# Optimization experiments

Measured on AMD Instinct MI355X. Metric: run time of the kernel, lower is better.

Reference implementation:

```python
import jax, jax.numpy as jnp
import numpy as np

H = 32       # total query heads
HK = 8       # kv heads (GQA)
D = 128      # head_dim = hidden // H
HIDDEN = 4096
THETA = 10000.0


def setup_inputs() -> dict:
    key = jax.random.key(0)
    k1, k2, k3 = jax.random.split(key, 3)
    B, S = 2, 2048
    positions = jnp.arange(S, dtype=jnp.int32)
    hidden_states = jax.random.normal(k1, (B, S, HIDDEN), dtype=jnp.float32)
    w_qkv = jax.random.normal(k2, (HIDDEN, (H + 2 * HK) * D), dtype=jnp.float32) * 0.02
    w_o = jax.random.normal(k3, (H * D, HIDDEN), dtype=jnp.float32) * 0.02
    return {"positions": positions, "hidden_states": hidden_states,
            "w_qkv": w_qkv, "w_o": w_o}


def _rope(x, cos, sin):
    # neox-style rotary: split halves, rotate
    x1, x2 = jnp.split(x, 2, axis=-1)
    return jnp.concatenate([x1 * cos - x2 * sin, x2 * cos + x1 * sin], axis=-1)


def reference(positions, hidden_states, w_qkv, w_o):
    B, S, _ = hidden_states.shape
    qkv = hidden_states @ w_qkv                        # [B,S,(H+2HK)*D]
    q, k, v = jnp.split(qkv, [H * D, H * D + HK * D], axis=-1)
    q = q.reshape(B, S, H, D)
    k = k.reshape(B, S, HK, D)
    v = v.reshape(B, S, HK, D)

    inv_freq = 1.0 / (THETA ** (jnp.arange(0, D, 2, dtype=jnp.float32) / D))
    freqs = positions.astype(jnp.float32)[:, None] * inv_freq[None, :]  # [S,D/2]
    cos = jnp.cos(freqs)[None, :, None, :]
    sin = jnp.sin(freqs)[None, :, None, :]
    q = _rope(q, cos, sin)
    k = _rope(k, cos, sin)

    G = H // HK  # query heads per kv head
    qg = q.reshape(B, S, HK, G, D)
    scores = jnp.einsum('bqhgd,bkhd->bhgqk', qg, k) * (D ** -0.5)
    causal = jnp.tril(jnp.ones((S, S), dtype=bool))
    scores = jnp.where(causal[None, None, None], scores, jnp.float32(-1e30))
    probs = jax.nn.softmax(scores, axis=-1)
    out = jnp.einsum('bhgqk,bkhd->bqhgd', probs, v).reshape(B, S, H * D)
    return out @ w_o
```

## Files before the change

kernel.cpp:

```cpp
#include <hip/hip_runtime.h>

typedef unsigned short ushort_t;
typedef __attribute__((ext_vector_type(8))) short short8;
typedef __attribute__((ext_vector_type(4))) unsigned short ushort4_t;
typedef __attribute__((ext_vector_type(4))) float f32x4;

#define NH 32
#define NHK 8
#define HD 128
#define HID 4096
#define NB 2
#define SEQ 2048
#define NQKV ((NH + 2 * NHK) * HD)

static __device__ inline ushort_t f2bu(float x) {
  unsigned u = __builtin_bit_cast(unsigned, x);
  unsigned r = (u + 0x7FFFu + ((u >> 16) & 1u)) >> 16;
  return (ushort_t)r;
}

typedef __attribute__((address_space(1))) void gvoid;
typedef __attribute__((address_space(3))) void lvoid;
static __device__ inline void gld16(const void* g, void* l) {
  __builtin_amdgcn_global_load_lds((gvoid*)g, (lvoid*)l, 16, 0, 0);
}

__global__ void rope_tab_k(const int* __restrict__ positions, float* __restrict__ tab) {
  int i = blockIdx.x * 256 + threadIdx.x;
  int s = i >> 6, d = i & 63;
  float pos = (float)positions[s];
  float f = pos * exp2f(-0.20762050593046014f * (float)d);
  tab[2 * i] = cosf(f);
  tab[2 * i + 1] = sinf(f);
}

__global__ void h2b_k(const float* __restrict__ in, ushort_t* __restrict__ out) {
  long i = ((long)blockIdx.x * 256 + threadIdx.x) * 8;
  f32x4 a = *(const f32x4*)&in[i];
  f32x4 b = *(const f32x4*)&in[i + 4];
  ushort4_t ya, yb;
#pragma unroll
  for (int u = 0; u < 4; ++u) { ya[u] = f2bu(a[u]); yb[u] = f2bu(b[u]); }
  *(ushort4_t*)&out[i] = ya;
  *(ushort4_t*)&out[i + 4] = yb;
}

__global__ void wt_k(const float* __restrict__ in, ushort_t* __restrict__ out,
                     int K, int N) {
  __shared__ ushort_t T[64][72];
  int n0 = blockIdx.x * 64, k0 = blockIdx.y * 64;
  int t = threadIdx.x;
  int kr = t >> 4, nc = (t & 15) * 4;
#pragma unroll
  for (int p = 0; p < 4; ++p) {
    int k = kr + p * 16;
    f32x4 x = *(const f32x4*)&in[(long)(k0 + k) * N + n0 + nc];
    ushort4_t y;
#pragma unroll
    for (int u = 0; u < 4; ++u) y[u] = f2bu(x[u]);
    *(ushort4_t*)&T[k][nc] = y;
  }
  __syncthreads();
  int n = t >> 2, kc = (t & 3) * 16;
  ushort_t tmp[16];
#pragma unroll
  for (int j = 0; j < 16; ++j) tmp[j] = T[kc + j][n];
  *(short8*)&out[(long)(n0 + n) * K + k0 + kc] = *(short8*)&tmp[0];
  *(short8*)&out[(long)(n0 + n) * K + k0 + kc + 8] = *(short8*)&tmp[8];
}

template <int MODE>
__global__ __launch_bounds__(256, 2)
void gemm_bt(const ushort_t* __restrict__ A,
             const ushort_t* __restrict__ Bt,
             float* __restrict__ C,
             const float* __restrict__ tab,
             ushort_t* __restrict__ Qo,
             ushort_t* __restrict__ Ko,
             ushort_t* __restrict__ Vo,
             int M, int N, int K) {
  __shared__ ushort_t As[2][128 * 32];
  __shared__ ushort_t Bs[2][128 * 32];
  int m0 = blockIdx.y * 128, n0 = blockIdx.x * 128;
  int tid = threadIdx.x;
  int lane = tid & 63, wave = tid >> 6;
  int wm = wave * 32;
  int l15 = lane & 15, quad = lane >> 4;
  f32x4 acc[2][8];
#pragma unroll
  for (int i = 0; i < 2; ++i)
#pragma unroll
    for (int j = 0; j < 8; ++j) acc[i][j] = (f32x4){0.f, 0.f, 0.f, 0.f};

  int iw = wave * 2;
  int r0 = iw * 16 + (lane >> 2);
  int gk0 = ((lane & 3) ^ ((r0 >> 1) & 3)) * 8;
  int r1 = r0 + 16;
  int gk1 = ((lane & 3) ^ ((r1 >> 1) & 3)) * 8;

#define STAGE(buf, k0)                                                   \
  do {                                                                   \
    gld16(&A[(long)(m0 + r0) * K + (k0) + gk0], &As[buf][iw * 512]);     \
    gld16(&Bt[(long)(n0 + r0) * K + (k0) + gk0], &Bs[buf][iw * 512]);    \
    gld16(&A[(long)(m0 + r1) * K + (k0) + gk1], &As[buf][iw * 512 + 512]); \
    gld16(&Bt[(long)(n0 + r1) * K + (k0) + gk1], &Bs[buf][iw * 512 + 512]); \
  } while (0)

  int NT = K >> 5;
  STAGE(0, 0);
  __syncthreads();
  int cur = 0;
  for (int t = 0; t < NT; ++t) {
    if (t + 1 < NT) STAGE(cur ^ 1, (t + 1) << 5);
    short8 af[2], bfr[8];
#pragma unroll
    for (int i = 0; i < 2; ++i) {
      int r = wm + i * 16 + l15;
      af[i] = *(short8*)&As[cur][r * 32 + ((quad ^ ((r >> 1) & 3)) << 3)];
    }
#pragma unroll
    for (int j = 0; j < 8; ++j) {
      int r = j * 16 + l15;
      bfr[j] = *(short8*)&Bs[cur][r * 32 + ((quad ^ ((r >> 1) & 3)) << 3)];
    }
#pragma unroll
    for (int i = 0; i < 2; ++i)
#pragma unroll
      for (int j = 0; j < 8; ++j)
        acc[i][j] = __builtin_amdgcn_mfma_f32_16x16x32_bf16(af[i], bfr[j], acc[i][j], 0, 0, 0);
    __syncthreads();
    cur ^= 1;
  }
#undef STAGE

  if (MODE == 0) {
#pragma unroll
    for (int i = 0; i < 2; ++i)
#pragma unroll
      for (int j = 0; j < 8; ++j)
#pragma unroll
        for (int r = 0; r < 4; ++r) {
          int row = m0 + wm + i * 16 + quad * 4 + r;
          int col = n0 + j * 16 + l15;
          C[(long)row * N + col] = acc[i][j][r];
        }
  } else {
    int head = n0 >> 7;
    const float2* tb = (const float2*)tab;
    if (head < NH + NHK) {
      bool isq = head < NH;
      ushort_t* dst = isq ? (Qo + (long)head * SEQ * HD)
                          : (Ko + (long)(head - NH) * SEQ * HD);
      float sc = isq ? 0.08838834764831845f : 1.0f;
#pragma unroll
      for (int i = 0; i < 2; ++i)
#pragma unroll
        for (int r = 0; r < 4; ++r) {
          int s = m0 + wm + i * 16 + quad * 4 + r;
#pragma unroll
          for (int j = 0; j < 4; ++j) {
            int d = j * 16 + l15;
            float2 cs = tb[s * 64 + d];
            float x1 = acc[i][j][r], x2 = acc[i][j + 4][r];
            dst[(long)s * HD + d] = f2bu((x1 * cs.x - x2 * cs.y) * sc);
            dst[(long)s * HD + d + 64] = f2bu((x2 * cs.x + x1 * cs.y) * sc);
          }
        }
    } else {
      int hk = head - NH - NHK;
      ushort_t* dst = Vo + (long)hk * HD * SEQ;
#pragma unroll
      for (int i = 0; i < 2; ++i)
#pragma unroll
        for (int j = 0; j < 8; ++j)
#pragma unroll
          for (int r = 0; r < 4; ++r) {
            int s = m0 + wm + i * 16 + quad * 4 + r;
            int d = j * 16 + l15;
            dst[(long)d * SEQ + s] = f2bu(acc[i][j][r]);
          }
    }
  }
}

template <int MODE, typename TA>
__global__ __launch_bounds__(256, 2)
void gemm_kn(const TA* __restrict__ A,
             const float* __restrict__ B,
             float* __restrict__ C,
             const float* __restrict__ tab,
             ushort_t* __restrict__ Qo,
             ushort_t* __restrict__ Ko,
             ushort_t* __restrict__ Vo,
             int M, int N, int K) {
  __shared__ ushort_t As[128][40];
  __shared__ ushort_t Bs[128 * 32];
  int m0 = blockIdx.y * 128, n0 = blockIdx.x * 128;
  int tid = threadIdx.x;
  int lane = tid & 63, wave = tid >> 6;
  int wm = wave * 32;
  int l15 = lane & 15, quad = lane >> 4;
  f32x4 acc[2][8];
#pragma unroll
  for (int i = 0; i < 2; ++i)
#pragma unroll
    for (int j = 0; j < 8; ++j) acc[i][j] = (f32x4){0.f, 0.f, 0.f, 0.f};

  for (int k0 = 0; k0 < K; k0 += 32) {
    __syncthreads();
    if constexpr (sizeof(TA) == 2) {
#pragma unroll
      for (int it = 0; it < 2; ++it) {
        int v = tid + it * 256;
        int row = v >> 2, kc = (v & 3) * 8;
        *(short8*)&As[row][kc] =
            *(const short8*)&A[(long)(m0 + row) * K + k0 + kc];
      }
    } else {
#pragma unroll
      for (int it = 0; it < 4; ++it) {
        int v = tid + it * 256;
        int row = v >> 3, kc = (v & 7) * 4;
        f32x4 x = *(const f32x4*)&A[(long)(m0 + row) * K + k0 + kc];
        ushort4_t y;
#pragma unroll
        for (int u = 0; u < 4; ++u) y[u] = f2bu(x[u]);
        *(ushort4_t*)&As[row][kc] = y;
      }
    }
#pragma unroll
    for (int it = 0; it < 4; ++it) {
      int v = tid + it * 256;
      int kr = v >> 5, nc = (v & 31) * 4;
      f32x4 x = *(const f32x4*)&B[(long)(k0 + kr) * N + n0 + nc];
      int kg = (kr >> 3) << 3, ke = kr & 7;
#pragma unroll
      for (int u = 0; u < 4; ++u) {
        int n = nc + u;
        Bs[n * 32 + ((kg ^ (((n >> 2) & 3) << 3))) + ke] = f2bu(x[u]);
      }
    }
    __syncthreads();
    short8 af[2], bfr[8];
#pragma unroll
    for (int i = 0; i < 2; ++i) af[i] = *(short8*)&As[wm + i * 16 + l15][quad * 8];
#pragma unroll
    for (int j = 0; j < 8; ++j) {
      int n = j * 16 + l15;
      bfr[j] = *(short8*)&Bs[n * 32 + ((quad ^ ((n >> 2) & 3)) << 3)];
    }
#pragma unroll
    for (int i = 0; i < 2; ++i)
#pragma unroll
      for (int j = 0; j < 8; ++j)
        acc[i][j] = __builtin_amdgcn_mfma_f32_16x16x32_bf16(af[i], bfr[j], acc[i][j], 0, 0, 0);
  }

  if (MODE == 0) {
#pragma unroll
    for (int i = 0; i < 2; ++i)
#pragma unroll
      for (int j = 0; j < 8; ++j)
#pragma unroll
        for (int r = 0; r < 4; ++r) {
          int row = m0 + wm + i * 16 + quad * 4 + r;
          int col = n0 + j * 16 + l15;
          C[(long)row * N + col] = acc[i][j][r];
        }
  } else {
    int head = n0 >> 7;
    const float2* tb = (const float2*)tab;
    if (head < NH + NHK) {
      bool isq = head < NH;
      ushort_t* dst = isq ? (Qo + (long)head * SEQ * HD)
                          : (Ko + (long)(head - NH) * SEQ * HD);
      float sc = isq ? 0.08838834764831845f : 1.0f;
#pragma unroll
      for (int i = 0; i < 2; ++i)
#pragma unroll
        for (int r = 0; r < 4; ++r) {
          int s = m0 + wm + i * 16 + quad * 4 + r;
#pragma unroll
          for (int j = 0; j < 4; ++j) {
            int d = j * 16 + l15;
            float2 cs = tb[s * 64 + d];
            float x1 = acc[i][j][r], x2 = acc[i][j + 4][r];
            dst[(long)s * HD + d] = f2bu((x1 * cs.x - x2 * cs.y) * sc);
            dst[(long)s * HD + d + 64] = f2bu((x2 * cs.x + x1 * cs.y) * sc);
          }
        }
    } else {
      int hk = head - NH - NHK;
      ushort_t* dst = Vo + (long)hk * HD * SEQ;
#pragma unroll
      for (int i = 0; i < 2; ++i)
#pragma unroll
        for (int j = 0; j < 8; ++j)
#pragma unroll
          for (int r = 0; r < 4; ++r) {
            int s = m0 + wm + i * 16 + quad * 4 + r;
            int d = j * 16 + l15;
            dst[(long)d * SEQ + s] = f2bu(acc[i][j][r]);
          }
    }
  }
}

__global__ __launch_bounds__(256, 2) void attn_k(const ushort_t* __restrict__ Q,
                                                 const ushort_t* __restrict__ Kg,
                                                 const ushort_t* __restrict__ Vt,
                                                 ushort_t* __restrict__ Aout) {
  __shared__ ushort_t Ks[64][136];
  __shared__ ushort_t Vs[128][72];
  __shared__ ushort_t Ps[4][16][72];
  int qt = ((int)gridDim.x - 1 - blockIdx.x) * 64;
  int h = blockIdx.y;
  int hk = h >> 2;
  const ushort_t* Qh = Q + (long)h * SEQ * HD;
  const ushort_t* Kh = Kg + (long)hk * SEQ * HD;
  const ushort_t* Vh = Vt + (long)hk * HD * SEQ;
  int tid = threadIdx.x, lane = tid & 63, wave = tid >> 6;
  int l15 = lane & 15, quad = lane >> 4;
  int qw = qt + wave * 16;
  short8 qf[4];
#pragma unroll
  for (int c = 0; c < 4; ++c)
    qf[c] = *(const short8*)&Qh[(long)(qw + l15) * HD + c * 32 + quad * 8];
  f32x4 O[8];
#pragma unroll
  for (int dt = 0; dt < 8; ++dt) O[dt] = (f32x4){0.f, 0.f, 0.f, 0.f};
  float mrow[4], lrow[4];
#pragma unroll
  for (int r = 0; r < 4; ++r) { mrow[r] = -1e30f; lrow[r] = 0.f; }
  int kend = qt + 64;
  for (int kc = 0; kc < kend; kc += 64) {
    __syncthreads();
#pragma unroll
    for (int i = 0; i < 4; ++i) {
      int v = tid + i * 256;
      int kr = v >> 4, dc = (v & 15) * 8;
      *(short8*)&Ks[kr][dc] = *(const short8*)&Kh[(long)(kc + kr) * HD + dc];
    }
#pragma unroll
    for (int i = 0; i < 4; ++i) {
      int v = tid + i * 256;
      int dr = v >> 3, kcol = (v & 7) * 8;
      *(short8*)&Vs[dr][kcol] = *(const short8*)&Vh[(long)dr * SEQ + kc + kcol];
    }
    __syncthreads();
    bool active = (kc <= qw + 15);
    if (active) {
      f32x4 S[4];
#pragma unroll
      for (int t = 0; t < 4; ++t) S[t] = (f32x4){0.f, 0.f, 0.f, 0.f};
#pragma unroll
      for (int c = 0; c < 4; ++c) {
#pragma unroll
        for (int t = 0; t < 4; ++t) {
          short8 kf = *(short8*)&Ks[t * 16 + l15][c * 32 + quad * 8];
          S[t] = __builtin_amdgcn_mfma_f32_16x16x32_bf16(qf[c], kf, S[t], 0, 0, 0);
        }
      }
#pragma unroll
      for (int r = 0; r < 4; ++r) {
        int qrow = qw + quad * 4 + r;
        float vv[4];
#pragma unroll
        for (int t = 0; t < 4; ++t)
          vv[t] = (kc + t * 16 + l15 <= qrow) ? S[t][r] : -1e30f;
        float mx = fmaxf(fmaxf(vv[0], vv[1]), fmaxf(vv[2], vv[3]));
        mx = fmaxf(mx, __shfl_xor(mx, 1, 64));
        mx = fmaxf(mx, __shfl_xor(mx, 2, 64));
        mx = fmaxf(mx, __shfl_xor(mx, 4, 64));
        mx = fmaxf(mx, __shfl_xor(mx, 8, 64));
        float mnew = fmaxf(mrow[r], mx);
        float alpha = __expf(mrow[r] - mnew);
        float p[4];
#pragma unroll
        for (int t = 0; t < 4; ++t) p[t] = __expf(vv[t] - mnew);
        float rs = (p[0] + p[1]) + (p[2] + p[3]);
        rs += __shfl_xor(rs, 1, 64);
        rs += __shfl_xor(rs, 2, 64);
        rs += __shfl_xor(rs, 4, 64);
        rs += __shfl_xor(rs, 8, 64);
        lrow[r] = lrow[r] * alpha + rs;
        mrow[r] = mnew;
#pragma unroll
        for (int dt = 0; dt < 8; ++dt) O[dt][r] *= alpha;
#pragma unroll
        for (int t = 0; t < 4; ++t)
          Ps[wave][quad * 4 + r][t * 16 + l15] = f2bu(p[t]);
      }
    }
    __syncthreads();
    if (active) {
      short8 pf0 = *(short8*)&Ps[wave][l15][quad * 8];
      short8 pf1 = *(short8*)&Ps[wave][l15][32 + quad * 8];
#pragma unroll
      for (int dt = 0; dt < 8; ++dt) {
        short8 vf0 = *(short8*)&Vs[dt * 16 + l15][quad * 8];
        short8 vf1 = *(short8*)&Vs[dt * 16 + l15][32 + quad * 8];
        O[dt] = __builtin_amdgcn_mfma_f32_16x16x32_bf16(pf0, vf0, O[dt], 0, 0, 0);
        O[dt] = __builtin_amdgcn_mfma_f32_16x16x32_bf16(pf1, vf1, O[dt], 0, 0, 0);
      }
    }
  }
#pragma unroll
  for (int dt = 0; dt < 8; ++dt)
#pragma unroll
    for (int r = 0; r < 4; ++r) {
      int q = qw + quad * 4 + r;
      float o = O[dt][r] / lrow[r];
      Aout[(long)q * (NH * HD) + h * HD + dt * 16 + l15] = f2bu(o);
    }
}

extern "C" void kernel_launch(void* const* d_in, const int* in_sizes, int n_in,
                              void* d_out, int out_size, void* d_ws, size_t ws_size,
                              hipStream_t stream) {
  const int* positions = (const int*)d_in[0];
  const float* hidden = (const float*)d_in[1];
  const float* w_qkv = (const float*)d_in[2];
  const float* w_o = (const float*)d_in[3];
  char* ws = (char*)d_ws;
  ushort_t* Qb = (ushort_t*)(ws + 0L);
  ushort_t* Kb = (ushort_t*)(ws + 16777216L);
  ushort_t* Vtb = (ushort_t*)(ws + 20971520L);
  ushort_t* attno = (ushort_t*)(ws + 25165824L);
  float* tab = (float*)attno;
  ushort_t* hb16 = (ushort_t*)(ws + 41943040L);
  ushort_t* wqkvT = (ushort_t*)(ws + 75497472L);
  ushort_t* woT = (ushort_t*)(ws + 125829120L);
  float* outf = (float*)d_out;
  bool big = ws_size >= 159383552ULL;

  if (big) {
    h2b_k<<<dim3((NB * SEQ * HID) / (256 * 8)), 256, 0, stream>>>(hidden, hb16);
    wt_k<<<dim3(NQKV / 64, HID / 64), 256, 0, stream>>>(w_qkv, wqkvT, HID, NQKV);
    wt_k<<<dim3(HID / 64, HID / 64), 256, 0, stream>>>(w_o, woT, HID, HID);
  }
  for (int b = 0; b < NB; ++b) {
    rope_tab_k<<<dim3((SEQ * 64) / 256), 256, 0, stream>>>(positions, tab);
    if (big) {
      gemm_bt<1><<<dim3(NQKV / 128, SEQ / 128), 256, 0, stream>>>(
          hb16 + (long)b * SEQ * HID, wqkvT, nullptr, tab, Qb, Kb, Vtb,
          SEQ, NQKV, HID);
    } else {
      gemm_kn<1, float><<<dim3(NQKV / 128, SEQ / 128), 256, 0, stream>>>(
          hidden + (long)b * SEQ * HID, w_qkv, nullptr, tab, Qb, Kb, Vtb,
          SEQ, NQKV, HID);
    }
    attn_k<<<dim3(SEQ / 64, NH), 256, 0, stream>>>(Qb, Kb, Vtb, attno);
    if (big) {
      gemm_bt<0><<<dim3(HID / 128, SEQ / 128), 256, 0, stream>>>(
          attno, woT, outf + (long)b * SEQ * HID, nullptr, nullptr, nullptr,
          nullptr, SEQ, HID, HID);
    } else {
      gemm_kn<0, ushort_t><<<dim3(HID / 128, SEQ / 128), 256, 0, stream>>>(
          attno, w_o, outf + (long)b * SEQ * HID, nullptr, nullptr, nullptr,
          nullptr, SEQ, HID, HID);
    }
  }
}
```

Before: 1.014 ms.

## Double-buffer K/V tile loads via registers and widen attention blocks to 128 queries

The attention kernel now runs 512 threads (8 waves) per block, covering 128 query rows, so each K/V tile staged in LDS serves twice as many queries. Global loads for the next K/V tile are prefetched into registers while the current tile is computed, then written to LDS at the start of the next iteration. MFMA sections are wrapped in s_setprio to favour matrix instructions. Register pressure rises from the two prefetch buffers, and with 128-row blocks the causal tail leaves more waves idle per block.

```diff
diff --git a/kernel.cpp b/kernel.cpp
--- a/kernel.cpp
+++ b/kernel.cpp
@@ -306,14 +306,14 @@
   }
 }
 
-__global__ __launch_bounds__(256, 2) void attn_k(const ushort_t* __restrict__ Q,
+__global__ __launch_bounds__(512, 2) void attn_k(const ushort_t* __restrict__ Q,
                                                  const ushort_t* __restrict__ Kg,
                                                  const ushort_t* __restrict__ Vt,
                                                  ushort_t* __restrict__ Aout) {
   __shared__ ushort_t Ks[64][136];
   __shared__ ushort_t Vs[128][72];
-  __shared__ ushort_t Ps[4][16][72];
-  int qt = ((int)gridDim.x - 1 - blockIdx.x) * 64;
+  __shared__ ushort_t Ps[8][16][72];
+  int qt = ((int)gridDim.x - 1 - blockIdx.x) * 128;
   int h = blockIdx.y;
   int hk = h >> 2;
   const ushort_t* Qh = Q + (long)h * SEQ * HD;
@@ -322,6 +322,28 @@
   int tid = threadIdx.x, lane = tid & 63, wave = tid >> 6;
   int l15 = lane & 15, quad = lane >> 4;
   int qw = qt + wave * 16;
+  int skr0 = tid >> 4, sdc0 = (tid & 15) * 8;
+  int skr1 = (tid + 512) >> 4, sdc1 = ((tid + 512) & 15) * 8;
+  int sdr0 = tid >> 3, skc0 = (tid & 7) * 8;
+  int sdr1 = (tid + 512) >> 3, skc1 = ((tid + 512) & 7) * 8;
+  short8 kra[2], vra[2], krb[2], vrb[2];
+
+#define LOADREG(KR, VR, kcc)                                              \
+  do {                                                                    \
+    KR[0] = *(const short8*)&Kh[(long)((kcc) + skr0) * HD + sdc0];        \
+    KR[1] = *(const short8*)&Kh[(long)((kcc) + skr1) * HD + sdc1];        \
+    VR[0] = *(const short8*)&Vh[(long)sdr0 * SEQ + (kcc) + skc0];         \
+    VR[1] = *(const short8*)&Vh[(long)sdr1 * SEQ + (kcc) + skc1];         \
+  } while (0)
+
+#define STORELDS(KR, VR)                                                  \
+  do {                                                                    \
+    *(short8*)&Ks[skr0][sdc0] = KR[0];                                    \
+    *(short8*)&Ks[skr1][sdc1] = KR[1];                                    \
+    *(short8*)&Vs[sdr0][skc0] = VR[0];                                    \
+    *(short8*)&Vs[sdr1][skc1] = VR[1];                                    \
+  } while (0)
+
   short8 qf[4];
 #pragma unroll
   for (int c = 0; c < 4; ++c)
@@ -332,79 +354,87 @@
   float mrow[4], lrow[4];
 #pragma unroll
   for (int r = 0; r < 4; ++r) { mrow[r] = -1e30f; lrow[r] = 0.f; }
-  int kend = qt + 64;
-  for (int kc = 0; kc < kend; kc += 64) {
-    __syncthreads();
-#pragma unroll
-    for (int i = 0; i < 4; ++i) {
-      int v = tid + i * 256;
-      int kr = v >> 4, dc = (v & 15) * 8;
-      *(short8*)&Ks[kr][dc] = *(const short8*)&Kh[(long)(kc + kr) * HD + dc];
-    }
-#pragma unroll
-    for (int i = 0; i < 4; ++i) {
-      int v = tid + i * 256;
-      int dr = v >> 3, kcol = (v & 7) * 8;
-      *(short8*)&Vs[dr][kcol] = *(const short8*)&Vh[(long)dr * SEQ + kc + kcol];
-    }
-    __syncthreads();
-    bool active = (kc <= qw + 15);
-    if (active) {
-      f32x4 S[4];
-#pragma unroll
-      for (int t = 0; t < 4; ++t) S[t] = (f32x4){0.f, 0.f, 0.f, 0.f};
-#pragma unroll
-      for (int c = 0; c < 4; ++c) {
-#pragma unroll
-        for (int t = 0; t < 4; ++t) {
-          short8 kf = *(short8*)&Ks[t * 16 + l15][c * 32 + quad * 8];
-          S[t] = __builtin_amdgcn_mfma_f32_16x16x32_bf16(qf[c], kf, S[t], 0, 0, 0);
-        }
-      }
-#pragma unroll
-      for (int r = 0; r < 4; ++r) {
-        int qrow = qw + quad * 4 + r;
-        float vv[4];
-#pragma unroll
-        for (int t = 0; t < 4; ++t)
-          vv[t] = (kc + t * 16 + l15 <= qrow) ? S[t][r] : -1e30f;
-        float mx = fmaxf(fmaxf(vv[0], vv[1]), fmaxf(vv[2], vv[3]));
-        mx = fmaxf(mx, __shfl_xor(mx, 1, 64));
-        mx = fmaxf(mx, __shfl_xor(mx, 2, 64));
-        mx = fmaxf(mx, __shfl_xor(mx, 4, 64));
-        mx = fmaxf(mx, __shfl_xor(mx, 8, 64));
-        float mnew = fmaxf(mrow[r], mx);
-        float alpha = __expf(mrow[r] - mnew);
-        float p[4];
-#pragma unroll
-        for (int t = 0; t < 4; ++t) p[t] = __expf(vv[t] - mnew);
-        float rs = (p[0] + p[1]) + (p[2] + p[3]);
-        rs += __shfl_xor(rs, 1, 64);
-        rs += __shfl_xor(rs, 2, 64);
-        rs += __shfl_xor(rs, 4, 64);
-        rs += __shfl_xor(rs, 8, 64);
-        lrow[r] = lrow[r] * alpha + rs;
-        mrow[r] = mnew;
-#pragma unroll
-        for (int dt = 0; dt < 8; ++dt) O[dt][r] *= alpha;
-#pragma unroll
-        for (int t = 0; t < 4; ++t)
-          Ps[wave][quad * 4 + r][t * 16 + l15] = f2bu(p[t]);
-      }
-    }
-    __syncthreads();
-    if (active) {
-      short8 pf0 = *(short8*)&Ps[wave][l15][quad * 8];
-      short8 pf1 = *(short8*)&Ps[wave][l15][32 + quad * 8];
-#pragma unroll
-      for (int dt = 0; dt < 8; ++dt) {
-        short8 vf0 = *(short8*)&Vs[dt * 16 + l15][quad * 8];
-        short8 vf1 = *(short8*)&Vs[dt * 16 + l15][32 + quad * 8];
-        O[dt] = __builtin_amdgcn_mfma_f32_16x16x32_bf16(pf0, vf0, O[dt], 0, 0, 0);
-        O[dt] = __builtin_amdgcn_mfma_f32_16x16x32_bf16(pf1, vf1, O[dt], 0, 0, 0);
-      }
-    }
-  }
+  int kend = qt + 128;
+
+#define COMPUTE(kcc)                                                        \
+  do {                                                                      \
+    bool active = ((kcc) <= qw + 15);                     \
+    if (active) {                                                           \
+      f32x4 S[4];                                                           \
+      _Pragma("unroll") for (int t = 0; t < 4; ++t)                         \
+          S[t] = (f32x4){0.f, 0.f, 0.f, 0.f};                               \
+      __builtin_amdgcn_s_setprio(1);                                        \
+      _Pragma("unroll") for (int c = 0; c < 4; ++c) {                       \
+        _Pragma("unroll") for (int t = 0; t < 4; ++t) {                     \
+          short8 kf = *(short8*)&Ks[t * 16 + l15][c * 32 + quad * 8];       \
+          S[t] = __builtin_amdgcn_mfma_f32_16x16x32_bf16(qf[c], kf, S[t], 0, 0, 0); \
+        }                                                                   \
+      }                                                                     \
+      __builtin_amdgcn_s_setprio(0);                                        \
+      _Pragma("unroll") for (int r = 0; r < 4; ++r) {                       \
+        int qrow = qw + quad * 4 + r;                                       \
+        float vv[4];                                                        \
+        _Pragma("unroll") for (int t = 0; t < 4; ++t)                       \
+            vv[t] = ((kcc) + t * 16 + l15 <= qrow) ? S[t][r] : -1e30f;      \
+        float mx = fmaxf(fmaxf(vv[0], vv[1]), fmaxf(vv[2], vv[3]));         \
+        mx = fmaxf(mx, __shfl_xor(mx, 1, 64));                              \
+        mx = fmaxf(mx, __shfl_xor(mx, 2, 64));                              \
+        mx = fmaxf(mx, __shfl_xor(mx, 4, 64));                              \
+        mx = fmaxf(mx, __shfl_xor(mx, 8, 64));                              \
+        float mnew = fmaxf(mrow[r], mx);                                    \
+        float alpha = __expf(mrow[r] - mnew);                               \
+        float p[4];                                                         \
+        _Pragma("unroll") for (int t = 0; t < 4; ++t)                       \
+            p[t] = __expf(vv[t] - mnew);                                    \
+        float rs = (p[0] + p[1]) + (p[2] + p[3]);                           \
+        rs += __shfl_xor(rs, 1, 64);                                        \
+        rs += __shfl_xor(rs, 2, 64);                                        \
+        rs += __shfl_xor(rs, 4, 64);                                        \
+        rs += __shfl_xor(rs, 8, 64);                                        \
+        lrow[r] = lrow[r] * alpha + rs;                                     \
+        mrow[r] = mnew;                                                     \
+        _Pragma("unroll") for (int dt = 0; dt < 8; ++dt) O[dt][r] *= alpha; \
+        _Pragma("unroll") for (int t = 0; t < 4; ++t)                       \
+            Ps[wave][quad * 4 + r][t * 16 + l15] = f2bu(p[t]);              \
+      }                                                                     \
+    }                                                                       \
+    __syncthreads();                       \
+    if (active) {                                                           \
+      short8 pf0 = *(short8*)&Ps[wave][l15][quad * 8];                      \
+      short8 pf1 = *(short8*)&Ps[wave][l15][32 + quad * 8];                 \
+      __builtin_amdgcn_s_setprio(1);                                        \
+      _Pragma("unroll") for (int dt = 0; dt < 8; ++dt) {                    \
+        short8 vf0 = *(short8*)&Vs[dt * 16 + l15][quad * 8];                \
+        short8 vf1 = *(short8*)&Vs[dt * 16 + l15][32 + quad * 8];           \
+        O[dt] = __builtin_amdgcn_mfma_f32_16x16x32_bf16(pf0, vf0, O[dt], 0, 0, 0); \
+        O[dt] = __builtin_amdgcn_mfma_f32_16x16x32_bf16(pf1, vf1, O[dt], 0, 0, 0); \
+      }                                                                     \
+      __builtin_amdgcn_s_setprio(0);                                        \
+    }                                                                       \
+  } while (0)
+
+  LOADREG(kra, vra, 0);
+  int kc = 0;
+  for (;;) {
+    __syncthreads();
+    STORELDS(kra, vra);
+    if (kc + 64 < kend) LOADREG(krb, vrb, kc + 64);
+    __syncthreads();
+    COMPUTE(kc);
+    kc += 64;
+    if (kc >= kend) break;
+    __syncthreads();
+    STORELDS(krb, vrb);
+    if (kc + 64 < kend) LOADREG(kra, vra, kc + 64);
+    __syncthreads();
+    COMPUTE(kc);
+    kc += 64;
+    if (kc >= kend) break;
+  }
+#undef LOADREG
+#undef STORELDS
+#undef COMPUTE
+
 #pragma unroll
   for (int dt = 0; dt < 8; ++dt)
 #pragma unroll
@@ -450,7 +480,7 @@
           hidden + (long)b * SEQ * HID, w_qkv, nullptr, tab, Qb, Kb, Vtb,
           SEQ, NQKV, HID);
     }
-    attn_k<<<dim3(SEQ / 64, NH), 256, 0, stream>>>(Qb, Kb, Vtb, attno);
+    attn_k<<<dim3(SEQ / 128, NH), 512, 0, stream>>>(Qb, Kb, Vtb, attno);
     if (big) {
       gemm_bt<0><<<dim3(HID / 128, SEQ / 128), 256, 0, stream>>>(
           attno, woT, outf + (long)b * SEQ * HID, nullptr, nullptr, nullptr,
```

Result: no change. 1.006 ms (-0.8%).

## Load K/V fragments directly from global in attention, dropping LDS staging and barriers

Applied to the files above, without the earlier changes.

The attention kernel stops staging K and V tiles in shared memory behind block-wide barriers. Each wave now reads its MFMA operands for K and V straight from global memory, relying on the caches for reuse across the four waves. Each wave also stops at its own causal end instead of the block's. The kernel raises the occupancy hint in launch bounds and brackets the MFMA sections with s_setprio. This removes barrier stalls and idle causal iterations, but puts global-load latency directly in front of the MFMAs and gives up explicit sharing of K/V tiles between waves.

```diff
diff --git a/kernel.cpp b/kernel.cpp
--- a/kernel.cpp
+++ b/kernel.cpp
@@ -306,12 +306,10 @@
   }
 }
 
-__global__ __launch_bounds__(256, 2) void attn_k(const ushort_t* __restrict__ Q,
+__global__ __launch_bounds__(256, 4) void attn_k(const ushort_t* __restrict__ Q,
                                                  const ushort_t* __restrict__ Kg,
                                                  const ushort_t* __restrict__ Vt,
                                                  ushort_t* __restrict__ Aout) {
-  __shared__ ushort_t Ks[64][136];
-  __shared__ ushort_t Vs[128][72];
   __shared__ ushort_t Ps[4][16][72];
   int qt = ((int)gridDim.x - 1 - blockIdx.x) * 64;
   int h = blockIdx.y;
@@ -332,79 +330,65 @@
   float mrow[4], lrow[4];
 #pragma unroll
   for (int r = 0; r < 4; ++r) { mrow[r] = -1e30f; lrow[r] = 0.f; }
-  int kend = qt + 64;
-  for (int kc = 0; kc < kend; kc += 64) {
-    __syncthreads();
-#pragma unroll
-    for (int i = 0; i < 4; ++i) {
-      int v = tid + i * 256;
-      int kr = v >> 4, dc = (v & 15) * 8;
-      *(short8*)&Ks[kr][dc] = *(const short8*)&Kh[(long)(kc + kr) * HD + dc];
-    }
-#pragma unroll
-    for (int i = 0; i < 4; ++i) {
-      int v = tid + i * 256;
-      int dr = v >> 3, kcol = (v & 7) * 8;
-      *(short8*)&Vs[dr][kcol] = *(const short8*)&Vh[(long)dr * SEQ + kc + kcol];
-    }
-    __syncthreads();
-    bool active = (kc <= qw + 15);
-    if (active) {
-      f32x4 S[4];
-#pragma unroll
-      for (int t = 0; t < 4; ++t) S[t] = (f32x4){0.f, 0.f, 0.f, 0.f};
-#pragma unroll
-      for (int c = 0; c < 4; ++c) {
-#pragma unroll
-        for (int t = 0; t < 4; ++t) {
-          short8 kf = *(short8*)&Ks[t * 16 + l15][c * 32 + quad * 8];
-          S[t] = __builtin_amdgcn_mfma_f32_16x16x32_bf16(qf[c], kf, S[t], 0, 0, 0);
-        }
+  int mykend = qw + 16;
+
+  for (int kc = 0; kc < mykend; kc += 64) {
+    f32x4 S[4];
+#pragma unroll
+    for (int t = 0; t < 4; ++t) S[t] = (f32x4){0.f, 0.f, 0.f, 0.f};
+    __builtin_amdgcn_s_setprio(1);
+#pragma unroll
+    for (int c = 0; c < 4; ++c) {
+#pragma unroll
+      for (int t = 0; t < 4; ++t) {
+        short8 kf = *(const short8*)&Kh[(long)(kc + t * 16 + l15) * HD + c * 32 + quad * 8];
+        S[t] = __builtin_amdgcn_mfma_f32_16x16x32_bf16(qf[c], kf, S[t], 0, 0, 0);
       }
-#pragma unroll
-      for (int r = 0; r < 4; ++r) {
-        int qrow = qw + quad * 4 + r;
-        float vv[4];
-#pragma unroll
-        for (int t = 0; t < 4; ++t)
-          vv[t] = (kc + t * 16 + l15 <= qrow) ? S[t][r] : -1e30f;
-        float mx = fmaxf(fmaxf(vv[0], vv[1]), fmaxf(vv[2], vv[3]));
-        mx = fmaxf(mx, __shfl_xor(mx, 1, 64));
-        mx = fmaxf(mx, __shfl_xor(mx, 2, 64));
-        mx = fmaxf(mx, __shfl_xor(mx, 4, 64));
-        mx = fmaxf(mx, __shfl_xor(mx, 8, 64));
-        float mnew = fmaxf(mrow[r], mx);
-        float alpha = __expf(mrow[r] - mnew);
-        float p[4];
-#pragma unroll
-        for (int t = 0; t < 4; ++t) p[t] = __expf(vv[t] - mnew);
-        float rs = (p[0] + p[1]) + (p[2] + p[3]);
-        rs += __shfl_xor(rs, 1, 64);
-        rs += __shfl_xor(rs, 2, 64);
-        rs += __shfl_xor(rs, 4, 64);
-        rs += __shfl_xor(rs, 8, 64);
-        lrow[r] = lrow[r] * alpha + rs;
-        mrow[r] = mnew;
-#pragma unroll
-        for (int dt = 0; dt < 8; ++dt) O[dt][r] *= alpha;
-#pragma unroll
-        for (int t = 0; t < 4; ++t)
-          Ps[wave][quad * 4 + r][t * 16 + l15] = f2bu(p[t]);
-      }
-    }
-    __syncthreads();
-    if (active) {
-      short8 pf0 = *(short8*)&Ps[wave][l15][quad * 8];
-      short8 pf1 = *(short8*)&Ps[wave][l15][32 + quad * 8];
-#pragma unroll
-      for (int dt = 0; dt < 8; ++dt) {
-        short8 vf0 = *(short8*)&Vs[dt * 16 + l15][quad * 8];
-        short8 vf1 = *(short8*)&Vs[dt * 16 + l15][32 + quad * 8];
-        O[dt] = __builtin_amdgcn_mfma_f32_16x16x32_bf16(pf0, vf0, O[dt], 0, 0, 0);
-        O[dt] = __builtin_amdgcn_mfma_f32_16x16x32_bf16(pf1, vf1, O[dt], 0, 0, 0);
-      }
-    }
-  }
+    }
+    __builtin_amdgcn_s_setprio(0);
+#pragma unroll
+    for (int r = 0; r < 4; ++r) {
+      int qrow = qw + quad * 4 + r;
+      float vv[4];
+#pragma unroll
+      for (int t = 0; t < 4; ++t)
+        vv[t] = (kc + t * 16 + l15 <= qrow) ? S[t][r] : -1e30f;
+      float mx = fmaxf(fmaxf(vv[0], vv[1]), fmaxf(vv[2], vv[3]));
+      mx = fmaxf(mx, __shfl_xor(mx, 1, 64));
+      mx = fmaxf(mx, __shfl_xor(mx, 2, 64));
+      mx = fmaxf(mx, __shfl_xor(mx, 4, 64));
+      mx = fmaxf(mx, __shfl_xor(mx, 8, 64));
+      float mnew = fmaxf(mrow[r], mx);
+      float alpha = __expf(mrow[r] - mnew);
+      float p[4];
+#pragma unroll
+      for (int t = 0; t < 4; ++t) p[t] = __expf(vv[t] - mnew);
+      float rs = (p[0] + p[1]) + (p[2] + p[3]);
+      rs += __shfl_xor(rs, 1, 64);
+      rs += __shfl_xor(rs, 2, 64);
+      rs += __shfl_xor(rs, 4, 64);
+      rs += __shfl_xor(rs, 8, 64);
+      lrow[r] = lrow[r] * alpha + rs;
+      mrow[r] = mnew;
+#pragma unroll
+      for (int dt = 0; dt < 8; ++dt) O[dt][r] *= alpha;
+#pragma unroll
+      for (int t = 0; t < 4; ++t)
+        Ps[wave][quad * 4 + r][t * 16 + l15] = f2bu(p[t]);
+    }
+    short8 pf0 = *(short8*)&Ps[wave][l15][quad * 8];
+    short8 pf1 = *(short8*)&Ps[wave][l15][32 + quad * 8];
+    __builtin_amdgcn_s_setprio(1);
+#pragma unroll
+    for (int dt = 0; dt < 8; ++dt) {
+      short8 vf0 = *(const short8*)&Vh[(long)(dt * 16 + l15) * SEQ + kc + quad * 8];
+      short8 vf1 = *(const short8*)&Vh[(long)(dt * 16 + l15) * SEQ + kc + 32 + quad * 8];
+      O[dt] = __builtin_amdgcn_mfma_f32_16x16x32_bf16(pf0, vf0, O[dt], 0, 0, 0);
+      O[dt] = __builtin_amdgcn_mfma_f32_16x16x32_bf16(pf1, vf1, O[dt], 0, 0, 0);
+    }
+    __builtin_amdgcn_s_setprio(0);
+  }
+
 #pragma unroll
   for (int dt = 0; dt < 8; ++dt)
 #pragma unroll
```

Measured after the change: 1.567 ms. +54.5%, slower.
